# Optimization experiments

Measured on AMD Instinct MI355X. Metric: run time of the kernel, lower is better.

## Reference

```python
import jax, jax.numpy as jnp
import numpy as np

B, T = 512, 64
STOCH, DETER, HIDDEN = 32, 512, 512
ACT_DIM, EMBED = 12, 1024
MIN_STD = 0.1
LN_EPS = 1e-3


def _ln(x, g, b):
    m = x.mean(-1, keepdims=True)
    v = ((x - m) ** 2).mean(-1, keepdims=True)
    return (x - m) / jnp.sqrt(v + LN_EPS) * g + b


def setup_inputs() -> dict:
    key = jax.random.key(0)
    ks = jax.random.split(key, 12)

    def w(k, shape):
        fan_in = shape[0]
        return jax.random.normal(k, shape, jnp.float32) / np.sqrt(fan_in)

    is_first = jnp.zeros((B, T), jnp.float32).at[:, 0].set(1.0)
    return {
        "embed": jax.random.normal(ks[0], (B, T, EMBED), jnp.float32),
        "action": jax.random.normal(ks[1], (B, T, ACT_DIM), jnp.float32),
        "is_first": is_first,
        "eps_prior": jax.random.normal(ks[2], (B, T, STOCH), jnp.float32),
        "eps_post": jax.random.normal(ks[3], (B, T, STOCH), jnp.float32),
        "W_init": jax.random.normal(ks[4], (1, DETER), jnp.float32) * 0.02,
        "w_in": w(ks[5], (STOCH + ACT_DIM, HIDDEN)),
        "ln_in_g": jnp.ones((HIDDEN,), jnp.float32),
        "ln_in_b": jnp.zeros((HIDDEN,), jnp.float32),
        "w_gru": w(ks[6], (HIDDEN + DETER, 3 * DETER)),
        "ln_gru_g": jnp.ones((3 * DETER,), jnp.float32),
        "ln_gru_b": jnp.zeros((3 * DETER,), jnp.float32),
        "w_out": w(ks[7], (DETER, HIDDEN)),
        "ln_out_g": jnp.ones((HIDDEN,), jnp.float32),
        "ln_out_b": jnp.zeros((HIDDEN,), jnp.float32),
        "w_ims": w(ks[8], (HIDDEN, 2 * STOCH)),
        "b_ims": jnp.zeros((2 * STOCH,), jnp.float32),
        "w_obs": w(ks[9], (DETER + EMBED, HIDDEN)),
        "ln_obs_g": jnp.ones((HIDDEN,), jnp.float32),
        "ln_obs_b": jnp.zeros((HIDDEN,), jnp.float32),
        "w_ostat": w(ks[10], (HIDDEN, 2 * STOCH)),
        "b_ostat": jnp.zeros((2 * STOCH,), jnp.float32),
    }


def reference(embed, action, is_first, eps_prior, eps_post, W_init,
              w_in, ln_in_g, ln_in_b, w_gru, ln_gru_g, ln_gru_b,
              w_out, ln_out_g, ln_out_b, w_ims, b_ims,
              w_obs, ln_obs_g, ln_obs_b, w_ostat, b_ostat):
    # RSSM.observe with continuous stoch (discrete=False), mean_act='none',
    # std_act='softplus', initial='learned', rec_depth=1.
    def img_out_stats(deter):
        x = jax.nn.silu(_ln(deter @ w_out, ln_out_g, ln_out_b))
        s = x @ w_ims + b_ims
        mean = s[..., :STOCH]
        std = jax.nn.softplus(s[..., STOCH:]) + MIN_STD
        return mean, std

    bsz = embed.shape[0]
    deter0 = jnp.broadcast_to(jnp.tanh(W_init), (bsz, DETER))
    stoch0, _ = img_out_stats(deter0)  # mode of Normal = mean

    # time-major for scan
    eT = jnp.swapaxes(embed, 0, 1)
    aT = jnp.swapaxes(action, 0, 1)
    fT = jnp.swapaxes(is_first, 0, 1)[..., None]
    epT = jnp.swapaxes(eps_prior, 0, 1)
    eoT = jnp.swapaxes(eps_post, 0, 1)

    def step(carry, xs):
        stoch, deter = carry
        a, e, f, ep, eo = xs
        # is_first reset (blend with learned initial state)
        a = a * (1.0 - f)
        stoch = stoch * (1.0 - f) + stoch0 * f
        deter = deter * (1.0 - f) + deter0 * f
        # img_step
        x = jax.nn.silu(_ln(jnp.concatenate([stoch, a], -1) @ w_in, ln_in_g, ln_in_b))
        parts = _ln(jnp.concatenate([x, deter], -1) @ w_gru, ln_gru_g, ln_gru_b)
        r, c, u = jnp.split(parts, 3, -1)
        r = jax.nn.sigmoid(r)
        c = jnp.tanh(r * c)
        u = jax.nn.sigmoid(u - 1.0)  # update_bias = -1
        deter_n = u * c + (1.0 - u) * deter
        pm, ps = img_out_stats(deter_n)
        pstoch = pm + ps * ep  # reparameterized sample
        # obs_step posterior
        xo = jax.nn.silu(_ln(jnp.concatenate([deter_n, e], -1) @ w_obs, ln_obs_g, ln_obs_b))
        so = xo @ w_ostat + b_ostat
        om = so[..., :STOCH]
        ostd = jax.nn.softplus(so[..., STOCH:]) + MIN_STD
        ostoch = om + ostd * eo
        return (ostoch, deter_n), (ostoch, om, ostd, pstoch, pm, ps, deter_n)

    _, ys = jax.lax.scan(step, (stoch0, deter0), (aT, eT, fT, epT, eoT))
    # batch-major, concat post(stoch,mean,std) prior(stoch,mean,std) deter -> [B,T,6*STOCH+DETER]
    return jnp.concatenate([jnp.swapaxes(y, 0, 1) for y in ys], -1)
```

## Files before the change

### kernel.cpp

```cpp
#include <hip/hip_runtime.h>
#include <hip/hip_bf16.h>


typedef __attribute__((ext_vector_type(8))) short bf16x8;
typedef __attribute__((ext_vector_type(4))) float f32x4;

static __device__ __forceinline__ short f2b(float x){
  __hip_bfloat16 h = __float2bfloat16(x);
  return *reinterpret_cast<short*>(&h);
}
static __device__ __forceinline__ float b2f(short s){
  __hip_bfloat16 h = *reinterpret_cast<__hip_bfloat16*>(&s);
  return __bfloat162float(h);
}
static __device__ __forceinline__ float softplusf_(float x){
  return (x > 20.f) ? x : log1pf(expf(x));
}

static __device__ __forceinline__ float bsum(float v, float* red){
  int tid = threadIdx.x;
  __syncthreads();
  red[tid] = v; __syncthreads();
  for(int s = blockDim.x>>1; s>0; s>>=1){
    if(tid < s) red[tid] += red[tid+s];
    __syncthreads();
  }
  return red[0];
}

static __device__ __forceinline__ void stage8f(short* dst, const float* src){
  float4 f0 = *reinterpret_cast<const float4*>(src);
  float4 f1 = *reinterpret_cast<const float4*>(src+4);
  bf16x8 v;
  v[0]=f2b(f0.x); v[1]=f2b(f0.y); v[2]=f2b(f0.z); v[3]=f2b(f0.w);
  v[4]=f2b(f1.x); v[5]=f2b(f1.y); v[6]=f2b(f1.z); v[7]=f2b(f1.w);
  *reinterpret_cast<bf16x8*>(dst) = v;
}

__global__ __launch_bounds__(256) void k_wt(const float* __restrict__ wg,
    const float* __restrict__ wo, const float* __restrict__ wou,
    short* __restrict__ wgruT, short* __restrict__ wobsDT,
    short* __restrict__ wobsET, short* __restrict__ woutT){
  int i = blockIdx.x*256 + threadIdx.x;
  if(i < 1572864){ int n = i>>10, k = i&1023; wgruT[i] = f2b(wg[k*1536+n]); return; }
  i -= 1572864;
  if(i < 262144){ int n = i>>9, k = i&511; wobsDT[i] = f2b(wo[k*512+n]); return; }
  i -= 262144;
  if(i < 524288){ int n = i>>10, k = i&1023; wobsET[i] = f2b(wo[(512+k)*512+n]); return; }
  i -= 524288;
  { int n = i>>9, k = i&511; woutT[i] = f2b(wou[k*512+n]); }
}

__global__ __launch_bounds__(512) void k_init(const float* __restrict__ W_init,
    const float* __restrict__ w_out, const float* __restrict__ og, const float* __restrict__ ob,
    const float* __restrict__ w_ims, const float* __restrict__ b_ims,
    float* __restrict__ deter0, float* __restrict__ stoch0){
  __shared__ float d0[512]; __shared__ float red[512]; __shared__ float x2[512];
  int tid = threadIdx.x;
  float d = tanhf(W_init[tid]); d0[tid] = d; deter0[tid] = d; __syncthreads();
  float s = 0.f;
  for(int k=0;k<512;k++) s += d0[k]*w_out[k*512+tid];
  float sum = bsum(s, red);
  float sq  = bsum(s*s, red);
  float mu = sum/512.f, var = sq/512.f - mu*mu;
  float rstd = rsqrtf(var + 1e-3f);
  float xn = (s-mu)*rstd*og[tid] + ob[tid];
  float xs = xn/(1.f+expf(-xn));
  x2[tid] = xs; __syncthreads();
  if(tid < 32){
    float acc = b_ims[tid];
    for(int k=0;k<512;k++) acc += x2[k]*w_ims[k*64+tid];
    stoch0[tid] = acc;
  }
}

__global__ __launch_bounds__(256) void k_x0(const float* __restrict__ action,
    const float* __restrict__ is_first, const float* __restrict__ w_in,
    const float* __restrict__ ig, const float* __restrict__ ib,
    const float* __restrict__ deter0, const float* __restrict__ stoch0,
    short* __restrict__ xdeter, float* __restrict__ deterF){
  int b = blockIdx.x, tid = threadIdx.x;
  __shared__ float st[32]; __shared__ float al[12]; __shared__ float red[256];
  float f0 = is_first[b*64];
  if(tid < 32) st[tid] = stoch0[tid];
  if(tid < 12) al[tid] = action[b*768 + tid]*(1.f-f0);
  __syncthreads();
  float xp[2];
  for(int i=0;i<2;i++){
    int h = tid + i*256; float a = 0.f;
    for(int k=0;k<32;k++) a += st[k]*w_in[k*512+h];
    for(int k=0;k<12;k++) a += al[k]*w_in[(32+k)*512+h];
    xp[i] = a;
  }
  float sum = bsum(xp[0]+xp[1], red);
  float sq  = bsum(xp[0]*xp[0]+xp[1]*xp[1], red);
  float mu = sum/512.f, var = sq/512.f - mu*mu;
  float rstd = rsqrtf(var + 1e-3f);
  for(int i=0;i<2;i++){
    int h = tid + i*256;
    float xn = (xp[i]-mu)*rstd*ig[h]+ib[h];
    float xs = xn/(1.f+expf(-xn));
    xdeter[b*1024 + h] = f2b(xs);
    xdeter[b*1024 + 512 + h] = f2b(deter0[h]);
    deterF[b*512 + h] = deter0[h];
  }
}

__global__ __launch_bounds__(256) void k_gru(const short* __restrict__ Axd,
    const short* __restrict__ Bw, float* __restrict__ Cp){
  __shared__ __align__(16) short As[64][72];
  __shared__ __align__(16) short Bs[64][72];
  int tid = threadIdx.x, lane = tid&63, wid = tid>>6;
  int wm = (wid>>1)*32, wn = (wid&1)*32;
  int mP = blockIdx.x*64, nP = blockIdx.y*64;
  f32x4 acc[2][2] = {};
  for(int kt=0; kt<1024; kt+=64){
    #pragma unroll
    for(int c=0;c<2;c++){
      int idx = tid + c*256; int r = idx>>3, kc = (idx&7)*8;
      *(int4*)&As[r][kc] = *(const int4*)&Axd[(mP+r)*1024 + kt + kc];
      *(int4*)&Bs[r][kc] = *(const int4*)&Bw[(nP+r)*1024 + kt + kc];
    }
    __syncthreads();
    #pragma unroll
    for(int ks=0; ks<64; ks+=32){
      int ko = ks + 8*(lane>>4);
      bf16x8 a0 = *(const bf16x8*)&As[wm +      (lane&15)][ko];
      bf16x8 a1 = *(const bf16x8*)&As[wm + 16 + (lane&15)][ko];
      bf16x8 b0 = *(const bf16x8*)&Bs[wn +      (lane&15)][ko];
      bf16x8 b1 = *(const bf16x8*)&Bs[wn + 16 + (lane&15)][ko];
      acc[0][0] = __builtin_amdgcn_mfma_f32_16x16x32_bf16(a0,b0,acc[0][0],0,0,0);
      acc[0][1] = __builtin_amdgcn_mfma_f32_16x16x32_bf16(a0,b1,acc[0][1],0,0,0);
      acc[1][0] = __builtin_amdgcn_mfma_f32_16x16x32_bf16(a1,b0,acc[1][0],0,0,0);
      acc[1][1] = __builtin_amdgcn_mfma_f32_16x16x32_bf16(a1,b1,acc[1][1],0,0,0);
    }
    __syncthreads();
  }
  int r0 = (lane>>4)*4, c0 = lane&15;
  for(int mi=0;mi<2;mi++) for(int ni=0;ni<2;ni++){
    int row = mP + wm + mi*16 + r0, col = nP + wn + ni*16 + c0;
    #pragma unroll
    for(int r=0;r<4;r++) Cp[(row+r)*1536 + col] = acc[mi][ni][r];
  }
}

__global__ __launch_bounds__(256) void k_gates(const float* __restrict__ parts,
    const float* __restrict__ gg, const float* __restrict__ gb,
    const float* __restrict__ is_first, const float* __restrict__ deter0,
    float* __restrict__ deterF, short* __restrict__ deterB,
    float* __restrict__ out, int t){
  int b = blockIdx.x, tid = threadIdx.x;
  __shared__ float red[256];
  const float* p = parts + b*1536;
  float v[6]; float s=0.f, sq=0.f;
  #pragma unroll
  for(int k=0;k<6;k++){ v[k] = p[tid + k*256]; s += v[k]; sq += v[k]*v[k]; }
  float sum = bsum(s, red);
  float ssq = bsum(sq, red);
  float mu = sum/1536.f, var = ssq/1536.f - mu*mu;
  float rstd = rsqrtf(var + 1e-3f);
  float f = is_first[b*64 + t];
  for(int jj=0;jj<2;jj++){
    int j = tid + jj*256;
    float xr = (v[jj]  -mu)*rstd*gg[j]       + gb[j];
    float xc = (v[2+jj]-mu)*rstd*gg[512+j]   + gb[512+j];
    float xu = (v[4+jj]-mu)*rstd*gg[1024+j]  + gb[1024+j];
    float r = 1.f/(1.f+expf(-xr));
    float c = tanhf(r*xc);
    float u = 1.f/(1.f+expf(-(xu-1.f)));
    float dp = deterF[b*512+j]*(1.f-f) + deter0[j]*f;
    float dn = u*c + (1.f-u)*dp;
    deterF[b*512+j] = dn;
    deterB[b*512+j] = f2b(dn);
    out[b*45056 + t*704 + 192 + j] = dn;
  }
}

__global__ __launch_bounds__(256) void k_obs(const short* __restrict__ dB,
    const float* __restrict__ emb, const short* __restrict__ WdT,
    const short* __restrict__ WeT, float* __restrict__ xopre, int t){
  __shared__ __align__(16) short As[64][72];
  __shared__ __align__(16) short Bs[64][72];
  int tid = threadIdx.x, lane = tid&63, wid = tid>>6;
  int wm = (wid>>1)*32, wn = (wid&1)*32;
  int mP = blockIdx.x*64, nP = blockIdx.y*64;
  f32x4 acc[2][2] = {};
  for(int kt=0; kt<24; kt++){
    #pragma unroll
    for(int c=0;c<2;c++){
      int idx = tid + c*256; int r = idx>>3, kc = (idx&7)*8;
      if(kt < 8){
        *(int4*)&As[r][kc] = *(const int4*)&dB[(mP+r)*512 + kt*64 + kc];
        *(int4*)&Bs[r][kc] = *(const int4*)&WdT[(nP+r)*512 + kt*64 + kc];
      } else {
        stage8f(&As[r][kc], &emb[(mP+r)*65536 + t*1024 + (kt-8)*64 + kc]);
        *(int4*)&Bs[r][kc] = *(const int4*)&WeT[(nP+r)*1024 + (kt-8)*64 + kc];
      }
    }
    __syncthreads();
    #pragma unroll
    for(int ks=0; ks<64; ks+=32){
      int ko = ks + 8*(lane>>4);
      bf16x8 a0 = *(const bf16x8*)&As[wm +      (lane&15)][ko];
      bf16x8 a1 = *(const bf16x8*)&As[wm + 16 + (lane&15)][ko];
      bf16x8 b0 = *(const bf16x8*)&Bs[wn +      (lane&15)][ko];
      bf16x8 b1 = *(const bf16x8*)&Bs[wn + 16 + (lane&15)][ko];
      acc[0][0] = __builtin_amdgcn_mfma_f32_16x16x32_bf16(a0,b0,acc[0][0],0,0,0);
      acc[0][1] = __builtin_amdgcn_mfma_f32_16x16x32_bf16(a0,b1,acc[0][1],0,0,0);
      acc[1][0] = __builtin_amdgcn_mfma_f32_16x16x32_bf16(a1,b0,acc[1][0],0,0,0);
      acc[1][1] = __builtin_amdgcn_mfma_f32_16x16x32_bf16(a1,b1,acc[1][1],0,0,0);
    }
    __syncthreads();
  }
  int r0 = (lane>>4)*4, c0 = lane&15;
  for(int mi=0;mi<2;mi++) for(int ni=0;ni<2;ni++){
    int row = mP + wm + mi*16 + r0, col = nP + wn + ni*16 + c0;
    #pragma unroll
    for(int r=0;r<4;r++) xopre[(row+r)*512 + col] = acc[mi][ni][r];
  }
}

__global__ __launch_bounds__(256) void k_post(const float* __restrict__ xopre,
    const float* __restrict__ og, const float* __restrict__ ob,
    const float* __restrict__ w_ostat, const float* __restrict__ b_ostat,
    const float* __restrict__ eps_post, const float* __restrict__ is_first,
    const float* __restrict__ action, const float* __restrict__ w_in,
    const float* __restrict__ ig, const float* __restrict__ ib,
    const float* __restrict__ stoch0, const float* __restrict__ deter0,
    const float* __restrict__ deterF, short* __restrict__ xdeter,
    float* __restrict__ out, int t){
  int b = blockIdx.x, tid = threadIdx.x;
  __shared__ float red[256]; __shared__ float xo[512];
  __shared__ float psh[4][64]; __shared__ float sol[64];
  __shared__ float st[32]; __shared__ float al[12];
  float xv[2];
  for(int i=0;i<2;i++) xv[i] = xopre[b*512 + tid + i*256];
  float sum = bsum(xv[0]+xv[1], red);
  float sq  = bsum(xv[0]*xv[0]+xv[1]*xv[1], red);
  float mu = sum/512.f, var = sq/512.f - mu*mu;
  float rstd = rsqrtf(var + 1e-3f);
  for(int i=0;i<2;i++){
    int h = tid + i*256;
    float xn = (xv[i]-mu)*rstd*og[h]+ob[h];
    xo[h] = xn/(1.f+expf(-xn));
  }
  __syncthreads();
  { int p = tid>>6, n = tid&63; float a = 0.f;
    for(int k=p*128; k<p*128+128; k++) a += xo[k]*w_ostat[k*64+n];
    psh[p][n] = a; }
  __syncthreads();
  if(tid < 64) sol[tid] = psh[0][tid]+psh[1][tid]+psh[2][tid]+psh[3][tid] + b_ostat[tid];
  __syncthreads();
  float fn = (t < 63) ? is_first[b*64 + t + 1] : 0.f;
  if(tid < 32){
    float om = sol[tid];
    float osd = softplusf_(sol[32+tid]) + 0.1f;
    float eo = eps_post[(b*64+t)*32 + tid];
    float ost = om + osd*eo;
    int base = b*45056 + t*704;
    out[base+tid] = ost; out[base+32+tid] = om; out[base+64+tid] = osd;
    st[tid] = ost*(1.f-fn) + stoch0[tid]*fn;
  }
  if(tid < 12 && t < 63) al[tid] = action[(b*64+t+1)*12 + tid]*(1.f-fn);
  __syncthreads();
  if(t < 63){
    float xp[2];
    for(int i=0;i<2;i++){
      int h = tid + i*256; float a = 0.f;
      for(int k=0;k<32;k++) a += st[k]*w_in[k*512+h];
      for(int k=0;k<12;k++) a += al[k]*w_in[(32+k)*512+h];
      xp[i] = a;
    }
    float s2 = bsum(xp[0]+xp[1], red);
    float q2 = bsum(xp[0]*xp[0]+xp[1]*xp[1], red);
    float mu2 = s2/512.f, var2 = q2/512.f - mu2*mu2;
    float rstd2 = rsqrtf(var2 + 1e-3f);
    for(int i=0;i<2;i++){
      int h = tid + i*256;
      float xn = (xp[i]-mu2)*rstd2*ig[h]+ib[h];
      float xs = xn/(1.f+expf(-xn));
      xdeter[b*1024 + h] = f2b(xs);
      xdeter[b*1024 + 512 + h] = f2b(deterF[b*512+h]*(1.f-fn) + deter0[h]*fn);
    }
  }
}

__global__ __launch_bounds__(256) void k_img(const float* __restrict__ outp,
    const short* __restrict__ WoT, short* __restrict__ x2pre){
  __shared__ __align__(16) short As[128][72];
  __shared__ __align__(16) short Bs[128][72];
  int tid = threadIdx.x, lane = tid&63, wid = tid>>6;
  int wm = (wid>>1)*64, wn = (wid&1)*64;
  int mP = blockIdx.x*128, nP = blockIdx.y*128;
  f32x4 acc[4][4] = {};
  for(int kt=0; kt<512; kt+=64){
    #pragma unroll
    for(int c=0;c<4;c++){
      int idx = tid + c*256; int r = idx>>3, kc = (idx&7)*8;
      stage8f(&As[r][kc], &outp[(mP+r)*704 + 192 + kt + kc]);
      *(int4*)&Bs[r][kc] = *(const int4*)&WoT[(nP+r)*512 + kt + kc];
    }
    __syncthreads();
    #pragma unroll
    for(int ks=0; ks<64; ks+=32){
      int ko = ks + 8*(lane>>4);
      bf16x8 a[4], b[4];
      #pragma unroll
      for(int i=0;i<4;i++){
        a[i] = *(const bf16x8*)&As[wm + i*16 + (lane&15)][ko];
        b[i] = *(const bf16x8*)&Bs[wn + i*16 + (lane&15)][ko];
      }
      #pragma unroll
      for(int mi=0;mi<4;mi++)
        #pragma unroll
        for(int ni=0;ni<4;ni++)
          acc[mi][ni] = __builtin_amdgcn_mfma_f32_16x16x32_bf16(a[mi],b[ni],acc[mi][ni],0,0,0);
    }
    __syncthreads();
  }
  int r0 = (lane>>4)*4, c0 = lane&15;
  for(int mi=0;mi<4;mi++) for(int ni=0;ni<4;ni++){
    int row = mP + wm + mi*16 + r0, col = nP + wn + ni*16 + c0;
    #pragma unroll
    for(int r=0;r<4;r++) x2pre[(row+r)*512 + col] = f2b(acc[mi][ni][r]);
  }
}

__global__ __launch_bounds__(256) void k_imgpost(const short* __restrict__ x2pre,
    const float* __restrict__ og, const float* __restrict__ ob,
    const float* __restrict__ w_ims, const float* __restrict__ b_ims,
    const float* __restrict__ eps_prior, float* __restrict__ out){
  int tid = threadIdx.x;
  int g = tid>>5, l = tid&31;
  int rbase = blockIdx.x*8;
  __shared__ float x2[8][512]; __shared__ float sl[8][64];
  int row = rbase + g;
  float vals[16]; float s=0.f, sq=0.f;
  #pragma unroll
  for(int i=0;i<16;i++){
    int k = l + i*32;
    float v = b2f(x2pre[row*512+k]);
    vals[i] = v; s += v; sq += v*v;
  }
  #pragma unroll
  for(int m=1;m<32;m<<=1){ s += __shfl_xor(s, m); sq += __shfl_xor(sq, m); }
  float mu = s/512.f, var = sq/512.f - mu*mu;
  float rstd = rsqrtf(var + 1e-3f);
  #pragma unroll
  for(int i=0;i<16;i++){
    int k = l + i*32;
    float xn = (vals[i]-mu)*rstd*og[k]+ob[k];
    x2[g][k] = xn/(1.f+expf(-xn));
  }
  __syncthreads();
  { int q = tid>>6, n = tid&63;
    float a0=0.f, a1=0.f;
    for(int k=0;k<512;k++){
      float w = w_ims[k*64+n];
      a0 += x2[q][k]*w; a1 += x2[q+4][k]*w;
    }
    sl[q][n]=a0; sl[q+4][n]=a1; }
  __syncthreads();
  { int r = tid>>5, n = tid&31; int rw = rbase + r;
    float pm = sl[r][n] + b_ims[n];
    float psd = softplusf_(sl[r][n+32] + b_ims[n+32]) + 0.1f;
    float ep = eps_prior[rw*32+n];
    int base = rw*704;
    out[base+96+n] = pm + psd*ep; out[base+128+n] = pm; out[base+160+n] = psd; }
}

extern "C" void kernel_launch(void* const* d_in, const int* in_sizes, int n_in,
                              void* d_out, int out_size, void* d_ws, size_t ws_size,
                              hipStream_t stream) {
  const float* embed     = (const float*)d_in[0];
  const float* action    = (const float*)d_in[1];
  const float* is_first  = (const float*)d_in[2];
  const float* eps_prior = (const float*)d_in[3];
  const float* eps_post  = (const float*)d_in[4];
  const float* W_init    = (const float*)d_in[5];
  const float* w_in      = (const float*)d_in[6];
  const float* ln_in_g   = (const float*)d_in[7];
  const float* ln_in_b   = (const float*)d_in[8];
  const float* w_gru     = (const float*)d_in[9];
  const float* ln_gru_g  = (const float*)d_in[10];
  const float* ln_gru_b  = (const float*)d_in[11];
  const float* w_out     = (const float*)d_in[12];
  const float* ln_out_g  = (const float*)d_in[13];
  const float* ln_out_b  = (const float*)d_in[14];
  const float* w_ims     = (const float*)d_in[15];
  const float* b_ims     = (const float*)d_in[16];
  const float* w_obs     = (const float*)d_in[17];
  const float* ln_obs_g  = (const float*)d_in[18];
  const float* ln_obs_b  = (const float*)d_in[19];
  const float* w_ostat   = (const float*)d_in[20];
  const float* b_ostat   = (const float*)d_in[21];
  float* out = (float*)d_out;
  char* ws = (char*)d_ws;

  short* wgruT  = (short*)(ws + 0);
  short* wobsDT = (short*)(ws + 3145728);
  short* wobsET = (short*)(ws + 3670016);
  short* woutT  = (short*)(ws + 4718592);
  float* deter0 = (float*)(ws + 5242880);
  float* stoch0 = (float*)(ws + 5244928);
  short* xdeter = (short*)(ws + 5245184);
  float* parts  = (float*)(ws + 6293760);
  float* deterF = (float*)(ws + 9439488);
  short* deterB = (short*)(ws + 10488064);
  float* xopre  = (float*)(ws + 11012352);
  short* x2pre  = (short*)(ws + 12060928);

  dim3 blk(256);
  hipLaunchKernelGGL(k_wt, dim3(10240), blk, 0, stream,
                     w_gru, w_obs, w_out, wgruT, wobsDT, wobsET, woutT);
  hipLaunchKernelGGL(k_init, dim3(1), dim3(512), 0, stream,
                     W_init, w_out, ln_out_g, ln_out_b, w_ims, b_ims, deter0, stoch0);
  hipLaunchKernelGGL(k_x0, dim3(512), blk, 0, stream,
                     action, is_first, w_in, ln_in_g, ln_in_b, deter0, stoch0, xdeter, deterF);
  for(int t=0; t<64; t++){
    hipLaunchKernelGGL(k_gru, dim3(8,24), blk, 0, stream, xdeter, wgruT, parts);
    hipLaunchKernelGGL(k_gates, dim3(512), blk, 0, stream,
                       parts, ln_gru_g, ln_gru_b, is_first, deter0, deterF, deterB, out, t);
    hipLaunchKernelGGL(k_obs, dim3(8,8), blk, 0, stream,
                       deterB, embed, wobsDT, wobsET, xopre, t);
    hipLaunchKernelGGL(k_post, dim3(512), blk, 0, stream,
                       xopre, ln_obs_g, ln_obs_b, w_ostat, b_ostat, eps_post, is_first,
                       action, w_in, ln_in_g, ln_in_b, stoch0, deter0, deterF, xdeter, out, t);
  }
  hipLaunchKernelGGL(k_img, dim3(256,4), blk, 0, stream, out, woutT, x2pre);
  hipLaunchKernelGGL(k_imgpost, dim3(4096), blk, 0, stream,
                     x2pre, ln_out_g, ln_out_b, w_ims, b_ims, eps_prior, out);
}
```

Before: 5.789 ms.

## Fuse recurrent scan into one persistent cooperative kernel with grid syncs

Replaces the 256 per-timestep kernel launches (GRU GEMM, gates, obs GEMM, posterior) with a single cooperative kernel of 256 blocks that loops over time and separates phases with grid.sync(). It also split-Ks the obs GEMM three ways (deter half plus two embed halves) so 192 blocks share the work, and the three partial results are summed in the posterior phase. The aim is to remove launch overhead and raise parallelism in the small obs GEMM. The cost is four grid-wide barriers per step and blocks idling during the GEMM phases. If the cooperative launch fails, it falls back to separate launches.

```diff
diff --git a/kernel.cpp b/kernel.cpp
--- a/kernel.cpp
+++ b/kernel.cpp
@@ -1,5 +1,7 @@
 #include <hip/hip_runtime.h>
 #include <hip/hip_bf16.h>
+#include <hip/hip_cooperative_groups.h>
+namespace cg = cooperative_groups;
 
 
 typedef __attribute__((ext_vector_type(8))) short bf16x8;
@@ -21,7 +23,7 @@
   int tid = threadIdx.x;
   __syncthreads();
   red[tid] = v; __syncthreads();
-  for(int s = blockDim.x>>1; s>0; s>>=1){
+  for(int s = 128; s>0; s>>=1){
     if(tid < s) red[tid] += red[tid+s];
     __syncthreads();
   }
@@ -37,89 +39,27 @@
   *reinterpret_cast<bf16x8*>(dst) = v;
 }
 
-__global__ __launch_bounds__(256) void k_wt(const float* __restrict__ wg,
-    const float* __restrict__ wo, const float* __restrict__ wou,
-    short* __restrict__ wgruT, short* __restrict__ wobsDT,
-    short* __restrict__ wobsET, short* __restrict__ woutT){
-  int i = blockIdx.x*256 + threadIdx.x;
-  if(i < 1572864){ int n = i>>10, k = i&1023; wgruT[i] = f2b(wg[k*1536+n]); return; }
-  i -= 1572864;
-  if(i < 262144){ int n = i>>9, k = i&511; wobsDT[i] = f2b(wo[k*512+n]); return; }
-  i -= 262144;
-  if(i < 524288){ int n = i>>10, k = i&1023; wobsET[i] = f2b(wo[(512+k)*512+n]); return; }
-  i -= 524288;
-  { int n = i>>9, k = i&511; woutT[i] = f2b(wou[k*512+n]); }
-}
-
-__global__ __launch_bounds__(512) void k_init(const float* __restrict__ W_init,
-    const float* __restrict__ w_out, const float* __restrict__ og, const float* __restrict__ ob,
-    const float* __restrict__ w_ims, const float* __restrict__ b_ims,
-    float* __restrict__ deter0, float* __restrict__ stoch0){
-  __shared__ float d0[512]; __shared__ float red[512]; __shared__ float x2[512];
-  int tid = threadIdx.x;
-  float d = tanhf(W_init[tid]); d0[tid] = d; deter0[tid] = d; __syncthreads();
-  float s = 0.f;
-  for(int k=0;k<512;k++) s += d0[k]*w_out[k*512+tid];
-  float sum = bsum(s, red);
-  float sq  = bsum(s*s, red);
-  float mu = sum/512.f, var = sq/512.f - mu*mu;
-  float rstd = rsqrtf(var + 1e-3f);
-  float xn = (s-mu)*rstd*og[tid] + ob[tid];
-  float xs = xn/(1.f+expf(-xn));
-  x2[tid] = xs; __syncthreads();
-  if(tid < 32){
-    float acc = b_ims[tid];
-    for(int k=0;k<512;k++) acc += x2[k]*w_ims[k*64+tid];
-    stoch0[tid] = acc;
-  }
-}
-
-__global__ __launch_bounds__(256) void k_x0(const float* __restrict__ action,
-    const float* __restrict__ is_first, const float* __restrict__ w_in,
-    const float* __restrict__ ig, const float* __restrict__ ib,
-    const float* __restrict__ deter0, const float* __restrict__ stoch0,
-    short* __restrict__ xdeter, float* __restrict__ deterF){
-  int b = blockIdx.x, tid = threadIdx.x;
-  __shared__ float st[32]; __shared__ float al[12]; __shared__ float red[256];
-  float f0 = is_first[b*64];
-  if(tid < 32) st[tid] = stoch0[tid];
-  if(tid < 12) al[tid] = action[b*768 + tid]*(1.f-f0);
-  __syncthreads();
-  float xp[2];
-  for(int i=0;i<2;i++){
-    int h = tid + i*256; float a = 0.f;
-    for(int k=0;k<32;k++) a += st[k]*w_in[k*512+h];
-    for(int k=0;k<12;k++) a += al[k]*w_in[(32+k)*512+h];
-    xp[i] = a;
-  }
-  float sum = bsum(xp[0]+xp[1], red);
-  float sq  = bsum(xp[0]*xp[0]+xp[1]*xp[1], red);
-  float mu = sum/512.f, var = sq/512.f - mu*mu;
-  float rstd = rsqrtf(var + 1e-3f);
-  for(int i=0;i<2;i++){
-    int h = tid + i*256;
-    float xn = (xp[i]-mu)*rstd*ig[h]+ib[h];
-    float xs = xn/(1.f+expf(-xn));
-    xdeter[b*1024 + h] = f2b(xs);
-    xdeter[b*1024 + 512 + h] = f2b(deter0[h]);
-    deterF[b*512 + h] = deter0[h];
-  }
-}
-
-__global__ __launch_bounds__(256) void k_gru(const short* __restrict__ Axd,
-    const short* __restrict__ Bw, float* __restrict__ Cp){
-  __shared__ __align__(16) short As[64][72];
-  __shared__ __align__(16) short Bs[64][72];
+template<bool AF32>
+static __device__ __forceinline__ void gemm_tile(
+    const void* __restrict__ Ap, int lda,
+    const short* __restrict__ Bp, int ldb,
+    float* __restrict__ Cp, int ldc,
+    int mP, int nP, int kA0, int kB0, int nkt,
+    short (*As)[72], short (*Bs)[72])
+{
   int tid = threadIdx.x, lane = tid&63, wid = tid>>6;
   int wm = (wid>>1)*32, wn = (wid&1)*32;
-  int mP = blockIdx.x*64, nP = blockIdx.y*64;
   f32x4 acc[2][2] = {};
-  for(int kt=0; kt<1024; kt+=64){
+  for(int kt=0; kt<nkt; kt++){
     #pragma unroll
     for(int c=0;c<2;c++){
       int idx = tid + c*256; int r = idx>>3, kc = (idx&7)*8;
-      *(int4*)&As[r][kc] = *(const int4*)&Axd[(mP+r)*1024 + kt + kc];
-      *(int4*)&Bs[r][kc] = *(const int4*)&Bw[(nP+r)*1024 + kt + kc];
+      if(AF32){
+        stage8f(&As[r][kc], (const float*)Ap + (size_t)(mP+r)*lda + kA0 + kt*64 + kc);
+      } else {
+        *(int4*)&As[r][kc] = *(const int4*)((const short*)Ap + (size_t)(mP+r)*lda + kA0 + kt*64 + kc);
+      }
+      *(int4*)&Bs[r][kc] = *(const int4*)&Bp[(size_t)(nP+r)*ldb + kB0 + kt*64 + kc];
     }
     __syncthreads();
     #pragma unroll
@@ -140,23 +80,28 @@
   for(int mi=0;mi<2;mi++) for(int ni=0;ni<2;ni++){
     int row = mP + wm + mi*16 + r0, col = nP + wn + ni*16 + c0;
     #pragma unroll
-    for(int r=0;r<4;r++) Cp[(row+r)*1536 + col] = acc[mi][ni][r];
-  }
-}
-
-__global__ __launch_bounds__(256) void k_gates(const float* __restrict__ parts,
-    const float* __restrict__ gg, const float* __restrict__ gb,
-    const float* __restrict__ is_first, const float* __restrict__ deter0,
-    float* __restrict__ deterF, short* __restrict__ deterB,
-    float* __restrict__ out, int t){
-  int b = blockIdx.x, tid = threadIdx.x;
-  __shared__ float red[256];
-  const float* p = parts + b*1536;
-  float v[6]; float s=0.f, sq=0.f;
+    for(int r=0;r<4;r++) Cp[(size_t)(row+r)*ldc + col] = acc[mi][ni][r];
+  }
+}
+
+static __device__ __forceinline__ void dev_p1(int task,
+    const short* xdeter, const short* wgruT, float* parts,
+    short (*As)[72], short (*Bs)[72]){
+  int mP = (task&7)*64, nP = (task>>3)*64;
+  gemm_tile<false>(xdeter, 1024, wgruT, 1024, parts, 1536, mP, nP, 0, 0, 16, As, Bs);
+}
+
+static __device__ __forceinline__ void dev_p2(int b, int t,
+    const float* parts, const float* gg, const float* gb,
+    const float* is_first, const float* deter0,
+    float* deterF, short* deterB, float* out, float* red){
+  int tid = threadIdx.x;
+  const float* p = parts + (size_t)b*1536;
+  float v[6]; float sv=0.f, sqv=0.f;
   #pragma unroll
-  for(int k=0;k<6;k++){ v[k] = p[tid + k*256]; s += v[k]; sq += v[k]*v[k]; }
-  float sum = bsum(s, red);
-  float ssq = bsum(sq, red);
+  for(int k=0;k<6;k++){ float x = p[tid+k*256]; v[k]=x; sv+=x; sqv+=x*x; }
+  float sum = bsum(sv, red);
+  float ssq = bsum(sqv, red);
   float mu = sum/1536.f, var = ssq/1536.f - mu*mu;
   float rstd = rsqrtf(var + 1e-3f);
   float f = is_first[b*64 + t];
@@ -172,55 +117,234 @@
     float dn = u*c + (1.f-u)*dp;
     deterF[b*512+j] = dn;
     deterB[b*512+j] = f2b(dn);
-    out[b*45056 + t*704 + 192 + j] = dn;
-  }
-}
-
-__global__ __launch_bounds__(256) void k_obs(const short* __restrict__ dB,
-    const float* __restrict__ emb, const short* __restrict__ WdT,
-    const short* __restrict__ WeT, float* __restrict__ xopre, int t){
+    out[(size_t)b*45056 + t*704 + 192 + j] = dn;
+  }
+}
+
+static __device__ __forceinline__ void dev_p3(int task, int t,
+    const short* deterB, const float* embed,
+    const short* wobsDT, const short* wobsET, float* xopreP,
+    short (*As)[72], short (*Bs)[72]){
+  int s = task/64, tile = task%64;
+  int mP = (tile&7)*64, nP = (tile>>3)*64;
+  if(s == 0){
+    gemm_tile<false>(deterB, 512, wobsDT, 512, xopreP, 512, mP, nP, 0, 0, 8, As, Bs);
+  } else if(s == 1){
+    gemm_tile<true>(embed + (size_t)t*1024, 65536, wobsET, 1024,
+                    xopreP + 262144, 512, mP, nP, 0, 0, 8, As, Bs);
+  } else {
+    gemm_tile<true>(embed + (size_t)t*1024, 65536, wobsET, 1024,
+                    xopreP + 524288, 512, mP, nP, 512, 512, 8, As, Bs);
+  }
+}
+
+static __device__ __forceinline__ void dev_p4(int b, int t,
+    const float* xopreP, const float* og, const float* ob,
+    const float* w_ostat, const float* b_ostat,
+    const float* eps_post, const float* is_first,
+    const float* action, const float* w_in,
+    const float* ig, const float* ib,
+    const float* stoch0, const float* deter0,
+    const float* deterF, short* xdeter, float* out, float* S){
+  int tid = threadIdx.x;
+  float* red = S;
+  float* xo  = S + 256;
+  float (*psh)[64] = (float(*)[64])(S + 768);
+  float* sol = S + 1024;
+  float* st  = S + 1088;
+  float* al  = S + 1120;
+  float xv[2];
+  for(int i=0;i<2;i++){
+    int h = tid + i*256;
+    float a = xopreP[(size_t)b*512 + h]
+            + xopreP[262144 + (size_t)b*512 + h]
+            + xopreP[524288 + (size_t)b*512 + h];
+    xv[i] = a;
+  }
+  float sum = bsum(xv[0]+xv[1], red);
+  float sq  = bsum(xv[0]*xv[0]+xv[1]*xv[1], red);
+  float mu = sum/512.f, var = sq/512.f - mu*mu;
+  float rstd = rsqrtf(var + 1e-3f);
+  for(int i=0;i<2;i++){
+    int h = tid + i*256;
+    float xn = (xv[i]-mu)*rstd*og[h]+ob[h];
+    xo[h] = xn/(1.f+expf(-xn));
+  }
+  __syncthreads();
+  { int p = tid>>6, n = tid&63; float a = 0.f;
+    for(int k=p*128; k<p*128+128; k++) a += xo[k]*w_ostat[k*64+n];
+    psh[p][n] = a; }
+  __syncthreads();
+  if(tid < 64) sol[tid] = psh[0][tid]+psh[1][tid]+psh[2][tid]+psh[3][tid] + b_ostat[tid];
+  __syncthreads();
+  float fn = (t < 63) ? is_first[b*64 + t + 1] : 0.f;
+  if(tid < 32){
+    float om = sol[tid];
+    float osd = softplusf_(sol[32+tid]) + 0.1f;
+    float eo = eps_post[(size_t)(b*64+t)*32 + tid];
+    float ost = om + osd*eo;
+    size_t base = (size_t)b*45056 + t*704;
+    out[base+tid] = ost; out[base+32+tid] = om; out[base+64+tid] = osd;
+    st[tid] = ost*(1.f-fn) + stoch0[tid]*fn;
+  }
+  if(tid < 12 && t < 63) al[tid] = action[(size_t)(b*64+t+1)*12 + tid]*(1.f-fn);
+  __syncthreads();
+  if(t < 63){
+    float xp[2];
+    for(int i=0;i<2;i++){
+      int h = tid + i*256; float a = 0.f;
+      for(int k=0;k<32;k++) a += st[k]*w_in[k*512+h];
+      for(int k=0;k<12;k++) a += al[k]*w_in[(32+k)*512+h];
+      xp[i] = a;
+    }
+    float s2 = bsum(xp[0]+xp[1], red);
+    float q2 = bsum(xp[0]*xp[0]+xp[1]*xp[1], red);
+    float mu2 = s2/512.f, var2 = q2/512.f - mu2*mu2;
+    float rstd2 = rsqrtf(var2 + 1e-3f);
+    for(int i=0;i<2;i++){
+      int h = tid + i*256;
+      float xn = (xp[i]-mu2)*rstd2*ig[h]+ib[h];
+      float xs = xn/(1.f+expf(-xn));
+      xdeter[(size_t)b*1024 + h] = f2b(xs);
+      xdeter[(size_t)b*1024 + 512 + h] = f2b(deterF[b*512+h]*(1.f-fn) + deter0[h]*fn);
+    }
+  }
+  __syncthreads();
+}
+
+__global__ __launch_bounds__(256) void k_wt(const float* __restrict__ wg,
+    const float* __restrict__ wo, const float* __restrict__ wou,
+    short* __restrict__ wgruT, short* __restrict__ wobsDT,
+    short* __restrict__ wobsET, short* __restrict__ woutT){
+  int i = blockIdx.x*256 + threadIdx.x;
+  if(i < 1572864){ int n = i>>10, k = i&1023; wgruT[i] = f2b(wg[k*1536+n]); return; }
+  i -= 1572864;
+  if(i < 262144){ int n = i>>9, k = i&511; wobsDT[i] = f2b(wo[k*512+n]); return; }
+  i -= 262144;
+  if(i < 524288){ int n = i>>10, k = i&1023; wobsET[i] = f2b(wo[(512+k)*512+n]); return; }
+  i -= 524288;
+  { int n = i>>9, k = i&511; woutT[i] = f2b(wou[k*512+n]); }
+}
+
+__global__ __launch_bounds__(512) void k_init(const float* __restrict__ W_init,
+    const float* __restrict__ w_out, const float* __restrict__ og, const float* __restrict__ ob,
+    const float* __restrict__ w_ims, const float* __restrict__ b_ims,
+    float* __restrict__ deter0, float* __restrict__ stoch0){
+  __shared__ float d0[512]; __shared__ float red[512]; __shared__ float x2[512];
+  int tid = threadIdx.x;
+  float d = tanhf(W_init[tid]); d0[tid] = d; deter0[tid] = d; __syncthreads();
+  float s = 0.f;
+  for(int k=0;k<512;k++) s += d0[k]*w_out[k*512+tid];
+  red[tid] = s; __syncthreads();
+  for(int ss=256; ss>0; ss>>=1){ if(tid<ss) red[tid]+=red[tid+ss]; __syncthreads(); }
+  float sum = red[0]; __syncthreads();
+  red[tid] = s*s; __syncthreads();
+  for(int ss=256; ss>0; ss>>=1){ if(tid<ss) red[tid]+=red[tid+ss]; __syncthreads(); }
+  float sq = red[0];
+  float mu = sum/512.f, var = sq/512.f - mu*mu;
+  float rstd = rsqrtf(var + 1e-3f);
+  float xn = (s-mu)*rstd*og[tid] + ob[tid];
+  float xs = xn/(1.f+expf(-xn));
+  x2[tid] = xs; __syncthreads();
+  if(tid < 32){
+    float acc = b_ims[tid];
+    for(int k=0;k<512;k++) acc += x2[k]*w_ims[k*64+tid];
+    stoch0[tid] = acc;
+  }
+}
+
+__global__ __launch_bounds__(256) void k_x0(const float* __restrict__ action,
+    const float* __restrict__ is_first, const float* __restrict__ w_in,
+    const float* __restrict__ ig, const float* __restrict__ ib,
+    const float* __restrict__ deter0, const float* __restrict__ stoch0,
+    short* __restrict__ xdeter, float* __restrict__ deterF){
+  int b = blockIdx.x, tid = threadIdx.x;
+  __shared__ float st[32]; __shared__ float al[12]; __shared__ float red[256];
+  float f0 = is_first[b*64];
+  if(tid < 32) st[tid] = stoch0[tid];
+  if(tid < 12) al[tid] = action[b*768 + tid]*(1.f-f0);
+  __syncthreads();
+  float xp[2];
+  for(int i=0;i<2;i++){
+    int h = tid + i*256; float a = 0.f;
+    for(int k=0;k<32;k++) a += st[k]*w_in[k*512+h];
+    for(int k=0;k<12;k++) a += al[k]*w_in[(32+k)*512+h];
+    xp[i] = a;
+  }
+  float sum = bsum(xp[0]+xp[1], red);
+  float sq  = bsum(xp[0]*xp[0]+xp[1]*xp[1], red);
+  float mu = sum/512.f, var = sq/512.f - mu*mu;
+  float rstd = rsqrtf(var + 1e-3f);
+  for(int i=0;i<2;i++){
+    int h = tid + i*256;
+    float xn = (xp[i]-mu)*rstd*ig[h]+ib[h];
+    float xs = xn/(1.f+expf(-xn));
+    xdeter[b*1024 + h] = f2b(xs);
+    xdeter[b*1024 + 512 + h] = f2b(deter0[h]);
+    deterF[b*512 + h] = deter0[h];
+  }
+}
+
+__global__ void k_scan(
+    short* __restrict__ xdeter, const short* __restrict__ wgruT,
+    float* __restrict__ parts,
+    const float* __restrict__ gg, const float* __restrict__ gb,
+    const float* __restrict__ is_first, const float* __restrict__ deter0,
+    float* __restrict__ deterF, short* __restrict__ deterB,
+    const short* __restrict__ wobsDT, const short* __restrict__ wobsET,
+    const float* __restrict__ embed, float* __restrict__ xopreP,
+    const float* __restrict__ og, const float* __restrict__ ob,
+    const float* __restrict__ w_ostat, const float* __restrict__ b_ostat,
+    const float* __restrict__ eps_post, const float* __restrict__ action,
+    const float* __restrict__ w_in, const float* __restrict__ ig,
+    const float* __restrict__ ib, const float* __restrict__ stoch0,
+    float* __restrict__ out)
+{
+  cg::grid_group grid = cg::this_grid();
+  __shared__ __align__(16) char smem[2*64*72*2];
+  short (*As)[72] = (short(*)[72])smem;
+  short (*Bs)[72] = (short(*)[72])(smem + 64*72*2);
+  float* S = (float*)smem;
+  int bid = blockIdx.x;
+
+  for(int t=0; t<64; t++){
+    if(bid < 192) dev_p1(bid, xdeter, wgruT, parts, As, Bs);
+    grid.sync();
+    dev_p2(2*bid,   t, parts, gg, gb, is_first, deter0, deterF, deterB, out, S);
+    dev_p2(2*bid+1, t, parts, gg, gb, is_first, deter0, deterF, deterB, out, S);
+    grid.sync();
+    if(bid < 192) dev_p3(bid, t, deterB, embed, wobsDT, wobsET, xopreP, As, Bs);
+    grid.sync();
+    dev_p4(2*bid,   t, xopreP, og, ob, w_ostat, b_ostat, eps_post, is_first,
+           action, w_in, ig, ib, stoch0, deter0, deterF, xdeter, out, S);
+    dev_p4(2*bid+1, t, xopreP, og, ob, w_ostat, b_ostat, eps_post, is_first,
+           action, w_in, ig, ib, stoch0, deter0, deterF, xdeter, out, S);
+    grid.sync();
+  }
+}
+
+__global__ __launch_bounds__(256) void k_p1(const short* __restrict__ xdeter,
+    const short* __restrict__ wgruT, float* __restrict__ parts){
   __shared__ __align__(16) short As[64][72];
   __shared__ __align__(16) short Bs[64][72];
-  int tid = threadIdx.x, lane = tid&63, wid = tid>>6;
-  int wm = (wid>>1)*32, wn = (wid&1)*32;
-  int mP = blockIdx.x*64, nP = blockIdx.y*64;
-  f32x4 acc[2][2] = {};
-  for(int kt=0; kt<24; kt++){
-    #pragma unroll
-    for(int c=0;c<2;c++){
-      int idx = tid + c*256; int r = idx>>3, kc = (idx&7)*8;
-      if(kt < 8){
-        *(int4*)&As[r][kc] = *(const int4*)&dB[(mP+r)*512 + kt*64 + kc];
-        *(int4*)&Bs[r][kc] = *(const int4*)&WdT[(nP+r)*512 + kt*64 + kc];
-      } else {
-        stage8f(&As[r][kc], &emb[(mP+r)*65536 + t*1024 + (kt-8)*64 + kc]);
-        *(int4*)&Bs[r][kc] = *(const int4*)&WeT[(nP+r)*1024 + (kt-8)*64 + kc];
-      }
-    }
-    __syncthreads();
-    #pragma unroll
-    for(int ks=0; ks<64; ks+=32){
-      int ko = ks + 8*(lane>>4);
-      bf16x8 a0 = *(const bf16x8*)&As[wm +      (lane&15)][ko];
-      bf16x8 a1 = *(const bf16x8*)&As[wm + 16 + (lane&15)][ko];
-      bf16x8 b0 = *(const bf16x8*)&Bs[wn +      (lane&15)][ko];
-      bf16x8 b1 = *(const bf16x8*)&Bs[wn + 16 + (lane&15)][ko];
-      acc[0][0] = __builtin_amdgcn_mfma_f32_16x16x32_bf16(a0,b0,acc[0][0],0,0,0);
-      acc[0][1] = __builtin_amdgcn_mfma_f32_16x16x32_bf16(a0,b1,acc[0][1],0,0,0);
-      acc[1][0] = __builtin_amdgcn_mfma_f32_16x16x32_bf16(a1,b0,acc[1][0],0,0,0);
-      acc[1][1] = __builtin_amdgcn_mfma_f32_16x16x32_bf16(a1,b1,acc[1][1],0,0,0);
-    }
-    __syncthreads();
-  }
-  int r0 = (lane>>4)*4, c0 = lane&15;
-  for(int mi=0;mi<2;mi++) for(int ni=0;ni<2;ni++){
-    int row = mP + wm + mi*16 + r0, col = nP + wn + ni*16 + c0;
-    #pragma unroll
-    for(int r=0;r<4;r++) xopre[(row+r)*512 + col] = acc[mi][ni][r];
-  }
-}
-
-__global__ __launch_bounds__(256) void k_post(const float* __restrict__ xopre,
+  dev_p1(blockIdx.x, xdeter, wgruT, parts, As, Bs);
+}
+__global__ __launch_bounds__(256) void k_p2(const float* __restrict__ parts,
+    const float* __restrict__ gg, const float* __restrict__ gb,
+    const float* __restrict__ is_first, const float* __restrict__ deter0,
+    float* __restrict__ deterF, short* __restrict__ deterB,
+    float* __restrict__ out, int t){
+  __shared__ float red[256];
+  dev_p2(blockIdx.x, t, parts, gg, gb, is_first, deter0, deterF, deterB, out, red);
+}
+__global__ __launch_bounds__(256) void k_p3(const short* __restrict__ deterB,
+    const float* __restrict__ embed, const short* __restrict__ wobsDT,
+    const short* __restrict__ wobsET, float* __restrict__ xopreP, int t){
+  __shared__ __align__(16) short As[64][72];
+  __shared__ __align__(16) short Bs[64][72];
+  dev_p3(blockIdx.x, t, deterB, embed, wobsDT, wobsET, xopreP, As, Bs);
+}
+__global__ __launch_bounds__(256) void k_p4(const float* __restrict__ xopreP,
     const float* __restrict__ og, const float* __restrict__ ob,
     const float* __restrict__ w_ostat, const float* __restrict__ b_ostat,
     const float* __restrict__ eps_post, const float* __restrict__ is_first,
@@ -229,60 +353,9 @@
     const float* __restrict__ stoch0, const float* __restrict__ deter0,
     const float* __restrict__ deterF, short* __restrict__ xdeter,
     float* __restrict__ out, int t){
-  int b = blockIdx.x, tid = threadIdx.x;
-  __shared__ float red[256]; __shared__ float xo[512];
-  __shared__ float psh[4][64]; __shared__ float sol[64];
-  __shared__ float st[32]; __shared__ float al[12];
-  float xv[2];
-  for(int i=0;i<2;i++) xv[i] = xopre[b*512 + tid + i*256];
-  float sum = bsum(xv[0]+xv[1], red);
-  float sq  = bsum(xv[0]*xv[0]+xv[1]*xv[1], red);
-  float mu = sum/512.f, var = sq/512.f - mu*mu;
-  float rstd = rsqrtf(var + 1e-3f);
-  for(int i=0;i<2;i++){
-    int h = tid + i*256;
-    float xn = (xv[i]-mu)*rstd*og[h]+ob[h];
-    xo[h] = xn/(1.f+expf(-xn));
-  }
-  __syncthreads();
-  { int p = tid>>6, n = tid&63; float a = 0.f;
-    for(int k=p*128; k<p*128+128; k++) a += xo[k]*w_ostat[k*64+n];
-    psh[p][n] = a; }
-  __syncthreads();
-  if(tid < 64) sol[tid] = psh[0][tid]+psh[1][tid]+psh[2][tid]+psh[3][tid] + b_ostat[tid];
-  __syncthreads();
-  float fn = (t < 63) ? is_first[b*64 + t + 1] : 0.f;
-  if(tid < 32){
-    float om = sol[tid];
-    float osd = softplusf_(sol[32+tid]) + 0.1f;
-    float eo = eps_post[(b*64+t)*32 + tid];
-    float ost = om + osd*eo;
-    int base = b*45056 + t*704;
-    out[base+tid] = ost; out[base+32+tid] = om; out[base+64+tid] = osd;
-    st[tid] = ost*(1.f-fn) + stoch0[tid]*fn;
-  }
-  if(tid < 12 && t < 63) al[tid] = action[(b*64+t+1)*12 + tid]*(1.f-fn);
-  __syncthreads();
-  if(t < 63){
-    float xp[2];
-    for(int i=0;i<2;i++){
-      int h = tid + i*256; float a = 0.f;
-      for(int k=0;k<32;k++) a += st[k]*w_in[k*512+h];
-      for(int k=0;k<12;k++) a += al[k]*w_in[(32+k)*512+h];
-      xp[i] = a;
-    }
-    float s2 = bsum(xp[0]+xp[1], red);
-    float q2 = bsum(xp[0]*xp[0]+xp[1]*xp[1], red);
-    float mu2 = s2/512.f, var2 = q2/512.f - mu2*mu2;
-    float rstd2 = rsqrtf(var2 + 1e-3f);
-    for(int i=0;i<2;i++){
-      int h = tid + i*256;
-      float xn = (xp[i]-mu2)*rstd2*ig[h]+ib[h];
-      float xs = xn/(1.f+expf(-xn));
-      xdeter[b*1024 + h] = f2b(xs);
-      xdeter[b*1024 + 512 + h] = f2b(deterF[b*512+h]*(1.f-fn) + deter0[h]*fn);
-    }
-  }
+  __shared__ float S[1152];
+  dev_p4(blockIdx.x, t, xopreP, og, ob, w_ostat, b_ostat, eps_post, is_first,
+         action, w_in, ig, ib, stoch0, deter0, deterF, xdeter, out, S);
 }
 
 __global__ __launch_bounds__(256) void k_img(const float* __restrict__ outp,
@@ -297,7 +370,7 @@
     #pragma unroll
     for(int c=0;c<4;c++){
       int idx = tid + c*256; int r = idx>>3, kc = (idx&7)*8;
-      stage8f(&As[r][kc], &outp[(mP+r)*704 + 192 + kt + kc]);
+      stage8f(&As[r][kc], &outp[(size_t)(mP+r)*704 + 192 + kt + kc]);
       *(int4*)&Bs[r][kc] = *(const int4*)&WoT[(nP+r)*512 + kt + kc];
     }
     __syncthreads();
@@ -322,7 +395,7 @@
   for(int mi=0;mi<4;mi++) for(int ni=0;ni<4;ni++){
     int row = mP + wm + mi*16 + r0, col = nP + wn + ni*16 + c0;
     #pragma unroll
-    for(int r=0;r<4;r++) x2pre[(row+r)*512 + col] = f2b(acc[mi][ni][r]);
+    for(int r=0;r<4;r++) x2pre[(size_t)(row+r)*512 + col] = f2b(acc[mi][ni][r]);
   }
 }
 
@@ -339,7 +412,7 @@
   #pragma unroll
   for(int i=0;i<16;i++){
     int k = l + i*32;
-    float v = b2f(x2pre[row*512+k]);
+    float v = b2f(x2pre[(size_t)row*512+k]);
     vals[i] = v; s += v; sq += v*v;
   }
   #pragma unroll
@@ -364,8 +437,8 @@
   { int r = tid>>5, n = tid&31; int rw = rbase + r;
     float pm = sl[r][n] + b_ims[n];
     float psd = softplusf_(sl[r][n+32] + b_ims[n+32]) + 0.1f;
-    float ep = eps_prior[rw*32+n];
-    int base = rw*704;
+    float ep = eps_prior[(size_t)rw*32+n];
+    size_t base = (size_t)rw*704;
     out[base+96+n] = pm + psd*ep; out[base+128+n] = pm; out[base+160+n] = psd; }
 }
 
@@ -404,11 +477,11 @@
   float* deter0 = (float*)(ws + 5242880);
   float* stoch0 = (float*)(ws + 5244928);
   short* xdeter = (short*)(ws + 5245184);
-  float* parts  = (float*)(ws + 6293760);
-  float* deterF = (float*)(ws + 9439488);
-  short* deterB = (short*)(ws + 10488064);
-  float* xopre  = (float*)(ws + 11012352);
-  short* x2pre  = (short*)(ws + 12060928);
+  float* deterF = (float*)(ws + 6293760);
+  short* deterB = (short*)(ws + 7342336);
+  float* parts  = (float*)(ws + 7866624);
+  float* xopreP = (float*)(ws + 11012352);
+  short* x2pre  = (short*)(ws + 7866624);
 
   dim3 blk(256);
   hipLaunchKernelGGL(k_wt, dim3(10240), blk, 0, stream,
@@ -417,16 +490,32 @@
                      W_init, w_out, ln_out_g, ln_out_b, w_ims, b_ims, deter0, stoch0);
   hipLaunchKernelGGL(k_x0, dim3(512), blk, 0, stream,
                      action, is_first, w_in, ln_in_g, ln_in_b, deter0, stoch0, xdeter, deterF);
-  for(int t=0; t<64; t++){
-    hipLaunchKernelGGL(k_gru, dim3(8,24), blk, 0, stream, xdeter, wgruT, parts);
-    hipLaunchKernelGGL(k_gates, dim3(512), blk, 0, stream,
-                       parts, ln_gru_g, ln_gru_b, is_first, deter0, deterF, deterB, out, t);
-    hipLaunchKernelGGL(k_obs, dim3(8,8), blk, 0, stream,
-                       deterB, embed, wobsDT, wobsET, xopre, t);
-    hipLaunchKernelGGL(k_post, dim3(512), blk, 0, stream,
-                       xopre, ln_obs_g, ln_obs_b, w_ostat, b_ostat, eps_post, is_first,
-                       action, w_in, ln_in_g, ln_in_b, stoch0, deter0, deterF, xdeter, out, t);
-  }
+
+  void* args[] = {
+    (void*)&xdeter, (void*)&wgruT, (void*)&parts,
+    (void*)&ln_gru_g, (void*)&ln_gru_b,
+    (void*)&is_first, (void*)&deter0, (void*)&deterF, (void*)&deterB,
+    (void*)&wobsDT, (void*)&wobsET, (void*)&embed, (void*)&xopreP,
+    (void*)&ln_obs_g, (void*)&ln_obs_b, (void*)&w_ostat, (void*)&b_ostat,
+    (void*)&eps_post, (void*)&action, (void*)&w_in,
+    (void*)&ln_in_g, (void*)&ln_in_b, (void*)&stoch0, (void*)&out
+  };
+  hipError_t cerr = hipLaunchCooperativeKernel((void*)k_scan, dim3(256), dim3(256),
+                                               args, 0, stream);
+  if(cerr != hipSuccess){
+    (void)hipGetLastError();
+    for(int t=0; t<64; t++){
+      hipLaunchKernelGGL(k_p1, dim3(192), blk, 0, stream, xdeter, wgruT, parts);
+      hipLaunchKernelGGL(k_p2, dim3(512), blk, 0, stream,
+                         parts, ln_gru_g, ln_gru_b, is_first, deter0, deterF, deterB, out, t);
+      hipLaunchKernelGGL(k_p3, dim3(192), blk, 0, stream,
+                         deterB, embed, wobsDT, wobsET, xopreP, t);
+      hipLaunchKernelGGL(k_p4, dim3(512), blk, 0, stream,
+                         xopreP, ln_obs_g, ln_obs_b, w_ostat, b_ostat, eps_post, is_first,
+                         action, w_in, ln_in_g, ln_in_b, stoch0, deter0, deterF, xdeter, out, t);
+    }
+  }
+
   hipLaunchKernelGGL(k_img, dim3(256,4), blk, 0, stream, out, woutT, x2pre);
   hipLaunchKernelGGL(k_imgpost, dim3(4096), blk, 0, stream,
                      x2pre, ln_out_g, ln_out_b, w_ims, b_ims, eps_prior, out);
```

New measurement: 19.35 ms. +234.3%, slower.
